# Optimization experiments

Measured on AMD Instinct MI355X. Metric: run time of the kernel, lower is better.

Reference implementation:

```python
import jax, jax.numpy as jnp
import numpy as np

KERNEL = 15
PAD = (KERNEL - 1) // 2  # 7


def setup_inputs() -> dict:
    key = jax.random.key(0)
    # [B, C, H, W] image batch in [0, 1)
    x = jax.random.uniform(key, (16, 3, 512, 512), dtype=jnp.float32)
    return {"x": x}


def reference(x):
    # channel-wise min -> [B, 1, H, W]
    xm = jnp.min(x, axis=1, keepdims=True)
    # ReflectionPad2d(pad) == numpy/jnp 'reflect' (no edge repeat)
    xp = jnp.pad(xm, ((0, 0), (0, 0), (PAD, PAD), (PAD, PAD)), mode="reflect")
    # sliding-window min (morphological erosion), replaces unfold+min
    dark = jax.lax.reduce_window(
        xp,
        jnp.inf,
        jax.lax.min,
        window_dimensions=(1, 1, KERNEL, KERNEL),
        window_strides=(1, 1, 1, 1),
        padding="VALID",
    )
    return dark  # [B, 1, H, W]
```

## Files before the change

### kernel.cpp

```cpp
#include <hip/hip_runtime.h>

#define IMG 512
#define CH_STRIDE (IMG * IMG)
#define STRIP 32
#define HR    46

typedef __attribute__((ext_vector_type(8))) _Float16 half8;
typedef __attribute__((ext_vector_type(4))) _Float16 half4;

__device__ __forceinline__ float4 fmin4(float4 a, float4 b) {
    float4 r;
    r.x = fminf(a.x, b.x); r.y = fminf(a.y, b.y);
    r.z = fminf(a.z, b.z); r.w = fminf(a.w, b.w);
    return r;
}

__global__ __launch_bounds__(512)
void dark_fused(const float* __restrict__ x, float* __restrict__ out) {
    __shared__ _Float16 hm[HR][IMG];

    const int tid   = threadIdx.x;
    const int wave  = tid >> 6;
    const int lane  = tid & 63;
    const int strip = blockIdx.x;
    const int img   = blockIdx.y;
    const int r0    = strip * STRIP - 7;

    const float* xb = x + img * 3 * CH_STRIDE;

    for (int j = wave; j < HR; j += 8) {
        int gr = r0 + j;
        gr = gr < 0 ? -gr : (gr > IMG - 1 ? 2 * (IMG - 1) - gr : gr);
        const float* p = xb + gr * IMG + 8 * lane;

        float4 a0 = *(const float4*)(p),                 a1 = *(const float4*)(p + 4);
        float4 b0 = *(const float4*)(p + CH_STRIDE),     b1 = *(const float4*)(p + CH_STRIDE + 4);
        float4 c0 = *(const float4*)(p + 2 * CH_STRIDE), c1 = *(const float4*)(p + 2 * CH_STRIDE + 4);
        float4 v0 = fmin4(fmin4(a0, b0), c0);
        float4 v1 = fmin4(fmin4(a1, b1), c1);

        float w0 = v0.x, w1 = v0.y, w2 = v0.z, w3 = v0.w;
        float w4 = v1.x, w5 = v1.y, w6 = v1.z, w7 = v1.w;

        float P1 = fminf(w0, w1), P2 = fminf(P1, w2), P3 = fminf(P2, w3),
              P4 = fminf(P3, w4), P5 = fminf(P4, w5), P6 = fminf(P5, w6),
              M  = fminf(P6, w7);
        float S6 = fminf(w7, w6), S5 = fminf(S6, w5), S4 = fminf(S5, w4),
              S3 = fminf(S4, w3), S2 = fminf(S3, w2), S1 = fminf(S2, w1);

        float SL1 = __shfl_up(S1, 1), SL2 = __shfl_up(S2, 1), SL3 = __shfl_up(S3, 1),
              SL4 = __shfl_up(S4, 1), SL5 = __shfl_up(S5, 1), SL6 = __shfl_up(S6, 1),
              SL7 = __shfl_up(w7, 1);
        float PR0 = __shfl_down(w0, 1), PR1 = __shfl_down(P1, 1), PR2 = __shfl_down(P2, 1),
              PR3 = __shfl_down(P3, 1), PR4 = __shfl_down(P4, 1), PR5 = __shfl_down(P5, 1),
              PR6 = __shfl_down(P6, 1);

        half8 hv;
        hv[0] = (_Float16)fminf(SL1, M);
        hv[1] = (_Float16)fminf(SL2, fminf(M, PR0));
        hv[2] = (_Float16)fminf(SL3, fminf(M, PR1));
        hv[3] = (_Float16)fminf(SL4, fminf(M, PR2));
        hv[4] = (_Float16)fminf(SL5, fminf(M, PR3));
        hv[5] = (_Float16)fminf(SL6, fminf(M, PR4));
        hv[6] = (_Float16)fminf(SL7, fminf(M, PR5));
        hv[7] = (_Float16)fminf(M, PR6);
        *(half8*)&hm[j][8 * lane] = hv;
    }
    __syncthreads();

    const int c4 = tid & 127;
    const int rg = tid >> 7;
    const int jb = rg * 8;

    float4 w[22];
    #pragma unroll
    for (int i = 0; i < 22; ++i) {
        half4 h = *(half4*)&hm[jb + i][4 * c4];
        w[i] = make_float4((float)h[0], (float)h[1], (float)h[2], (float)h[3]);
    }

    #pragma unroll
    for (int i = 13; i >= 0; --i) w[i] = fmin4(w[i], w[i + 1]);

    float* ob = out + img * CH_STRIDE + (strip * STRIP + jb) * IMG + 4 * c4;
    *(float4*)(ob) = w[0];
    float4 pr = w[15];
    #pragma unroll
    for (int k = 1; k < 8; ++k) {
        *(float4*)(ob + k * IMG) = fmin4(w[k], pr);
        if (k < 7) pr = fmin4(pr, w[15 + k]);
    }
}

extern "C" void kernel_launch(void* const* d_in, const int* in_sizes, int n_in,
                              void* d_out, int out_size, void* d_ws, size_t ws_size,
                              hipStream_t stream) {
    const float* x = (const float*)d_in[0];
    float* out = (float*)d_out;
    dim3 grid(IMG / STRIP, 16);
    dark_fused<<<grid, dim3(512), 0, stream>>>(x, out);
}
```

Measured before the change: 19.03 us.

## Use 1024-thread blocks with 4 output rows per thread and remapped grid

Doubles the block size to 1024 threads so each thread computes 4 output rows instead of 8. The vertical min now loads 18 rows and shares a common 12-row min across the 4 outputs. The grid is flattened to 256 blocks with a remapped image/strip index, likely to spread consecutive blocks across images. The aim is more parallelism per block and fewer registers per thread. The cost is more redundant vertical half-row loads from LDS and larger blocks that may cut occupancy per CU.

```diff
diff --git a/kernel.cpp b/kernel.cpp
--- a/kernel.cpp
+++ b/kernel.cpp
@@ -4,6 +4,7 @@
 #define CH_STRIDE (IMG * IMG)
 #define STRIP 32
 #define HR    46
+#define NT    1024
 
 typedef __attribute__((ext_vector_type(8))) _Float16 half8;
 typedef __attribute__((ext_vector_type(4))) _Float16 half4;
@@ -15,20 +16,22 @@
     return r;
 }
 
-__global__ __launch_bounds__(512)
+__global__ __launch_bounds__(NT)
 void dark_fused(const float* __restrict__ x, float* __restrict__ out) {
     __shared__ _Float16 hm[HR][IMG];
 
-    const int tid   = threadIdx.x;
-    const int wave  = tid >> 6;
-    const int lane  = tid & 63;
-    const int strip = blockIdx.x;
-    const int img   = blockIdx.y;
+    const int tid  = threadIdx.x;
+    const int wave = tid >> 6;
+    const int lane = tid & 63;
+
+    const int bid   = blockIdx.x;
+    const int img   = 2 * (bid & 7) + (bid >> 7);
+    const int strip = (bid >> 3) & 15;
     const int r0    = strip * STRIP - 7;
 
     const float* xb = x + img * 3 * CH_STRIDE;
 
-    for (int j = wave; j < HR; j += 8) {
+    for (int j = wave; j < HR; j += 16) {
         int gr = r0 + j;
         gr = gr < 0 ? -gr : (gr > IMG - 1 ? 2 * (IMG - 1) - gr : gr);
         const float* p = xb + gr * IMG + 8 * lane;
@@ -69,27 +72,27 @@
     __syncthreads();
 
     const int c4 = tid & 127;
-    const int rg = tid >> 7;
-    const int jb = rg * 8;
+    const int jb = (tid >> 7) * 4;
 
-    float4 w[22];
+    float4 w[18];
     #pragma unroll
-    for (int i = 0; i < 22; ++i) {
+    for (int i = 0; i < 18; ++i) {
         half4 h = *(half4*)&hm[jb + i][4 * c4];
         w[i] = make_float4((float)h[0], (float)h[1], (float)h[2], (float)h[3]);
     }
 
-    #pragma unroll
-    for (int i = 13; i >= 0; --i) w[i] = fmin4(w[i], w[i + 1]);
+    float4 ca = fmin4(fmin4(w[3],  w[4]),  fmin4(w[5],  w[6]));
+    float4 cb = fmin4(fmin4(w[7],  w[8]),  fmin4(w[9],  w[10]));
+    float4 cc = fmin4(fmin4(w[11], w[12]), fmin4(w[13], w[14]));
+    float4 common = fmin4(ca, fmin4(cb, cc));
+    float4 p01 = fmin4(w[1], w[2]);
+    float4 s01 = fmin4(w[15], w[16]);
 
     float* ob = out + img * CH_STRIDE + (strip * STRIP + jb) * IMG + 4 * c4;
-    *(float4*)(ob) = w[0];
-    float4 pr = w[15];
-    #pragma unroll
-    for (int k = 1; k < 8; ++k) {
-        *(float4*)(ob + k * IMG) = fmin4(w[k], pr);
-        if (k < 7) pr = fmin4(pr, w[15 + k]);
-    }
+    *(float4*)(ob)           = fmin4(fmin4(w[0], p01), common);
+    *(float4*)(ob + IMG)     = fmin4(fmin4(p01, w[15]), common);
+    *(float4*)(ob + 2 * IMG) = fmin4(fmin4(w[2], s01), common);
+    *(float4*)(ob + 3 * IMG) = fmin4(fmin4(s01, w[17]), common);
 }
 
 extern "C" void kernel_launch(void* const* d_in, const int* in_sizes, int n_in,
@@ -97,6 +100,5 @@
                               hipStream_t stream) {
     const float* x = (const float*)d_in[0];
     float* out = (float*)d_out;
-    dim3 grid(IMG / STRIP, 16);
-    dark_fused<<<grid, dim3(512), 0, stream>>>(x, out);
+    dark_fused<<<dim3(256), dim3(NT), 0, stream>>>(x, out);
 }
```

After: 18.41 us. -3.2%, faster.

## Halve strip height, remap block order, and narrow vertical pass to float2

Applied to the files above, without the earlier changes.

Strip height drops from 32 to 16 rows, which doubles the block count to 512 and shrinks shared memory per block, so each of the many CUs gets more blocks and occupancy rises. The grid becomes 1-D with a custom mapping that interleaves images across block indices, and launch bounds now request 4 blocks per SM. The vertical pass now has each thread cover 2 columns instead of 4. The trade-off is more halo overhead: 30 row-passes per 16 output rows instead of 46 per 32, which means more redundant global reads and channel-min work.

```diff
diff --git a/kernel.cpp b/kernel.cpp
--- a/kernel.cpp
+++ b/kernel.cpp
@@ -2,11 +2,12 @@
 
 #define IMG 512
 #define CH_STRIDE (IMG * IMG)
-#define STRIP 32
-#define HR    46
+#define STRIP 16
+#define HR    30
+#define NT    512
 
 typedef __attribute__((ext_vector_type(8))) _Float16 half8;
-typedef __attribute__((ext_vector_type(4))) _Float16 half4;
+typedef __attribute__((ext_vector_type(2))) _Float16 half2v;
 
 __device__ __forceinline__ float4 fmin4(float4 a, float4 b) {
     float4 r;
@@ -14,16 +15,24 @@
     r.z = fminf(a.z, b.z); r.w = fminf(a.w, b.w);
     return r;
 }
+__device__ __forceinline__ float2 fmin2(float2 a, float2 b) {
+    float2 r;
+    r.x = fminf(a.x, b.x); r.y = fminf(a.y, b.y);
+    return r;
+}
 
-__global__ __launch_bounds__(512)
+__global__ __launch_bounds__(NT, 4)
 void dark_fused(const float* __restrict__ x, float* __restrict__ out) {
     __shared__ _Float16 hm[HR][IMG];
 
-    const int tid   = threadIdx.x;
-    const int wave  = tid >> 6;
-    const int lane  = tid & 63;
-    const int strip = blockIdx.x;
-    const int img   = blockIdx.y;
+    const int tid  = threadIdx.x;
+    const int wave = tid >> 6;
+    const int lane = tid & 63;
+
+    const int bid   = blockIdx.x;
+    const int q     = bid >> 3;
+    const int img   = 2 * (bid & 7) + (q >> 5);
+    const int strip = q & 31;
     const int r0    = strip * STRIP - 7;
 
     const float* xb = x + img * 3 * CH_STRIDE;
@@ -68,27 +77,26 @@
     }
     __syncthreads();
 
-    const int c4 = tid & 127;
-    const int rg = tid >> 7;
-    const int jb = rg * 8;
+    const int c2 = tid & 255;
+    const int jb = (tid >> 8) * 8;
 
-    float4 w[22];
+    float2 w[22];
     #pragma unroll
     for (int i = 0; i < 22; ++i) {
-        half4 h = *(half4*)&hm[jb + i][4 * c4];
-        w[i] = make_float4((float)h[0], (float)h[1], (float)h[2], (float)h[3]);
+        half2v h = *(half2v*)&hm[jb + i][2 * c2];
+        w[i] = make_float2((float)h[0], (float)h[1]);
     }
 
     #pragma unroll
-    for (int i = 13; i >= 0; --i) w[i] = fmin4(w[i], w[i + 1]);
+    for (int i = 13; i >= 0; --i) w[i] = fmin2(w[i], w[i + 1]);
 
-    float* ob = out + img * CH_STRIDE + (strip * STRIP + jb) * IMG + 4 * c4;
-    *(float4*)(ob) = w[0];
-    float4 pr = w[15];
+    float* ob = out + img * CH_STRIDE + (strip * STRIP + jb) * IMG + 2 * c2;
+    *(float2*)(ob) = w[0];
+    float2 pr = w[15];
     #pragma unroll
     for (int k = 1; k < 8; ++k) {
-        *(float4*)(ob + k * IMG) = fmin4(w[k], pr);
-        if (k < 7) pr = fmin4(pr, w[15 + k]);
+        *(float2*)(ob + k * IMG) = fmin2(w[k], pr);
+        if (k < 7) pr = fmin2(pr, w[15 + k]);
     }
 }
 
@@ -97,6 +105,5 @@
                               hipStream_t stream) {
     const float* x = (const float*)d_in[0];
     float* out = (float*)d_out;
-    dim3 grid(IMG / STRIP, 16);
-    dark_fused<<<grid, dim3(512), 0, stream>>>(x, out);
+    dark_fused<<<dim3(512), dim3(NT), 0, stream>>>(x, out);
 }
```

Result: slower. 20.93 us (+10.0%).
